# Performance work log

Measured on AMD Instinct MI355X. Metric: run time of the kernel, lower is better.

## Reference

```python
import jax, jax.numpy as jnp
import numpy as np

N_USER = 100000
N_ITEM = 100000
E = 1000000
D_IN = 64
D_OUT = 64


def setup_inputs() -> dict:
    key = jax.random.key(0)
    ks = jax.random.split(key, 10)
    scale = 1.0 / np.sqrt(D_IN)
    return {
        "feat_user": jax.random.normal(ks[0], (N_USER, D_IN), jnp.float32),
        "feat_item": jax.random.normal(ks[1], (N_ITEM, D_IN), jnp.float32),
        "src_clicks": jax.random.randint(ks[2], (E,), 0, N_USER),        # user ids
        "dst_clicks": jax.random.randint(ks[3], (E,), 0, N_ITEM),        # item ids
        "src_clicked_by": jax.random.randint(ks[4], (E,), 0, N_ITEM),    # item ids
        "dst_clicked_by": jax.random.randint(ks[5], (E,), 0, N_USER),    # user ids
        "W_clicks": jax.random.normal(ks[6], (D_OUT, D_IN), jnp.float32) * scale,
        "b_clicks": jax.random.normal(ks[7], (D_OUT,), jnp.float32) * scale,
        "W_clicked_by": jax.random.normal(ks[8], (D_OUT, D_IN), jnp.float32) * scale,
        "b_clicked_by": jax.random.normal(ks[9], (D_OUT,), jnp.float32) * scale,
    }


def _relation_mean(feat_src, W, b, src, dst, n_dst):
    # per-relation Linear on src features (nn.Linear: x @ W.T + b)
    Wh = feat_src @ W.T + b                                  # [N_src, D_OUT]
    # copy_u + mean: gather messages along edges, segment-mean at dst
    msum = jax.ops.segment_sum(Wh[src], dst, num_segments=n_dst)   # [n_dst, D_OUT]
    deg = jax.ops.segment_sum(jnp.ones(src.shape[0], jnp.float32), dst,
                              num_segments=n_dst)                   # [n_dst]
    return msum / jnp.maximum(deg, 1.0)[:, None]             # zero-degree dsts -> 0


def reference(feat_user, feat_item, src_clicks, dst_clicks,
              src_clicked_by, dst_clicked_by,
              W_clicks, b_clicks, W_clicked_by, b_clicked_by):
    # relation (user, clicks, item): messages land on item nodes
    h_item = _relation_mean(feat_user, W_clicks, b_clicks,
                            src_clicks, dst_clicks, N_ITEM)
    # relation (item, clicked_by, user): messages land on user nodes
    h_user = _relation_mean(feat_item, W_clicked_by, b_clicked_by,
                            src_clicked_by, dst_clicked_by, N_USER)
    # cross-relation 'sum' reducer: each ntype receives from exactly one relation here
    return (h_user, h_item)
```

## Files before the change

### kernel.cpp

```cpp
#include <hip/hip_runtime.h>

#define D 64
#define BSH 7
#define BK 128
#define NBK 1024
#define CAP 2048
#define CHUNK 4096
#define EPT (CHUNK / 256)
#define TILE 64

static __device__ __forceinline__ unsigned short f2bf(float x) {
    unsigned int u = __float_as_uint(x);
    unsigned int r = (u + 0x7FFFu + ((u >> 16) & 1u)) >> 16;
    return (unsigned short)r;
}
static __device__ __forceinline__ float bf2f(unsigned short h) {
    return __uint_as_float((unsigned int)h << 16);
}

__global__ __launch_bounds__(256) void linear_gemm(
    const float* __restrict__ feat_u, const float* __restrict__ feat_i,
    const float* __restrict__ W_c, const float* __restrict__ b_c,
    const float* __restrict__ W_cb, const float* __restrict__ b_cb,
    unsigned short* __restrict__ Whb_u, unsigned short* __restrict__ Whb_i,
    int n_user, int n_item) {
    const float* feat; const float* W; const float* bia; unsigned short* out; int n;
    if (blockIdx.y == 0) { feat = feat_u; W = W_c;  bia = b_c;  out = Whb_u; n = n_user; }
    else                 { feat = feat_i; W = W_cb; bia = b_cb; out = Whb_i; n = n_item; }
    int row0 = blockIdx.x * TILE;
    if (row0 >= n) return;
    __shared__ float FT[TILE * D];
    __shared__ float WT[D * 68];
    int t = threadIdx.x;
    int lr = t >> 4;
    int k4 = (t & 15) * 4;
    #pragma unroll
    for (int it = 0; it < 4; ++it) {
        int r = lr + it * 16;
        int grow = row0 + r; if (grow > n - 1) grow = n - 1;
        float4 f = *(const float4*)(feat + (size_t)grow * D + k4);
        *(float4*)(FT + r * D + k4) = f;
        float4 w = *(const float4*)(W + r * D + k4);
        WT[(k4 + 0) * 68 + r] = w.x;
        WT[(k4 + 1) * 68 + r] = w.y;
        WT[(k4 + 2) * 68 + r] = w.z;
        WT[(k4 + 3) * 68 + r] = w.w;
    }
    __syncthreads();
    int c0 = (t & 15) * 4;
    int r0 = (t >> 4) * 4;
    float4 bv = *(const float4*)(bia + c0);
    float acc[4][4];
    #pragma unroll
    for (int ri = 0; ri < 4; ++ri) {
        acc[ri][0] = bv.x; acc[ri][1] = bv.y; acc[ri][2] = bv.z; acc[ri][3] = bv.w;
    }
    #pragma unroll 4
    for (int k = 0; k < D; ++k) {
        float4 w = *(const float4*)(WT + k * 68 + c0);
        float f0 = FT[(r0 + 0) * D + k];
        float f1 = FT[(r0 + 1) * D + k];
        float f2 = FT[(r0 + 2) * D + k];
        float f3 = FT[(r0 + 3) * D + k];
        acc[0][0] = fmaf(f0, w.x, acc[0][0]); acc[0][1] = fmaf(f0, w.y, acc[0][1]);
        acc[0][2] = fmaf(f0, w.z, acc[0][2]); acc[0][3] = fmaf(f0, w.w, acc[0][3]);
        acc[1][0] = fmaf(f1, w.x, acc[1][0]); acc[1][1] = fmaf(f1, w.y, acc[1][1]);
        acc[1][2] = fmaf(f1, w.z, acc[1][2]); acc[1][3] = fmaf(f1, w.w, acc[1][3]);
        acc[2][0] = fmaf(f2, w.x, acc[2][0]); acc[2][1] = fmaf(f2, w.y, acc[2][1]);
        acc[2][2] = fmaf(f2, w.z, acc[2][2]); acc[2][3] = fmaf(f2, w.w, acc[2][3]);
        acc[3][0] = fmaf(f3, w.x, acc[3][0]); acc[3][1] = fmaf(f3, w.y, acc[3][1]);
        acc[3][2] = fmaf(f3, w.z, acc[3][2]); acc[3][3] = fmaf(f3, w.w, acc[3][3]);
    }
    #pragma unroll
    for (int ri = 0; ri < 4; ++ri) {
        int row = row0 + r0 + ri;
        if (row < n) {
            ushort4 o;
            o.x = f2bf(acc[ri][0]); o.y = f2bf(acc[ri][1]);
            o.z = f2bf(acc[ri][2]); o.w = f2bf(acc[ri][3]);
            *(ushort4*)(out + (size_t)row * D + c0) = o;
        }
    }
}

__global__ __launch_bounds__(256) void bucket_fill(
    const int* __restrict__ srcA, const int* __restrict__ dstA,
    const int* __restrict__ srcB, const int* __restrict__ dstB,
    int* __restrict__ bcur,
    unsigned int* __restrict__ ebufA, unsigned int* __restrict__ ebufB,
    int n_edges) {
    int rel = blockIdx.y;
    const int* src = rel ? srcB : srcA;
    const int* dst = rel ? dstB : dstA;
    int* bu = bcur + rel * NBK;
    unsigned int* ebuf = rel ? ebufB : ebufA;
    __shared__ int hist[NBK], lofs[NBK], lcur[NBK], runb[NBK];
    __shared__ unsigned int stage[CHUNK];
    __shared__ unsigned short sbkt[CHUNK];
    __shared__ int ps[256];
    int t = threadIdx.x;
    for (int i = t; i < NBK; i += 256) hist[i] = 0;
    __syncthreads();
    int base = blockIdx.x * CHUNK;
    int m = n_edges - base; if (m > CHUNK) m = CHUNK;
    unsigned int packed[EPT];
    int bk[EPT];
    #pragma unroll
    for (int j = 0; j < EPT; ++j) {
        int e = base + j * 256 + t;
        if (e < n_edges) {
            int d = dst[e];
            int s = src[e];
            bk[j] = ((unsigned)d) >> BSH;
            packed[j] = (unsigned int)s | (((unsigned int)d & (BK - 1)) << 24);
            atomicAdd(&hist[bk[j]], 1);
        } else bk[j] = -1;
    }
    __syncthreads();
    int a[4]; int s4 = 0;
    #pragma unroll
    for (int j = 0; j < 4; ++j) { a[j] = hist[4 * t + j]; s4 += a[j]; }
    ps[t] = s4;
    __syncthreads();
    for (int o = 1; o < 256; o <<= 1) {
        int x = (t >= o) ? ps[t - o] : 0;
        __syncthreads();
        ps[t] += x;
        __syncthreads();
    }
    int ex = ps[t] - s4;
    #pragma unroll
    for (int j = 0; j < 4; ++j) {
        lofs[4 * t + j] = ex; lcur[4 * t + j] = ex;
        ex += a[j];
    }
    __syncthreads();
    for (int b = t; b < NBK; b += 256) {
        int c = hist[b];
        runb[b] = c ? (b * CAP + atomicAdd(&bu[b], c)) : 0;
    }
    #pragma unroll
    for (int j = 0; j < EPT; ++j) {
        if (bk[j] >= 0) {
            int p = atomicAdd(&lcur[bk[j]], 1);
            stage[p] = packed[j];
            sbkt[p] = (unsigned short)bk[j];
        }
    }
    __syncthreads();
    for (int i = t; i < m; i += 256) {
        int b = sbkt[i];
        int pos = runb[b] + (i - lofs[b]);
        if ((unsigned)(pos - b * CAP) < CAP)
            ebuf[pos] = stage[i];
    }
}

__global__ __launch_bounds__(256) void bucket_gather(
    const unsigned short* __restrict__ Whb_u, const unsigned short* __restrict__ Whb_i,
    const unsigned int* __restrict__ ebufA, const unsigned int* __restrict__ ebufB,
    const int* __restrict__ bcur,
    float* __restrict__ h_user, float* __restrict__ h_item,
    int n_user, int n_item) {
    int rel = blockIdx.y;
    const unsigned short* Wh = rel ? Whb_u : Whb_i;
    const unsigned int* ebuf = rel ? ebufB : ebufA;
    float* out = rel ? h_item : h_user;
    int n = rel ? n_item : n_user;
    int b = blockIdx.x;
    int cnt = bcur[rel * NBK + b]; if (cnt > CAP) cnt = CAP;
    size_t base = (size_t)b * CAP;
    __shared__ unsigned int ssrc[CAP];
    __shared__ int hist[BK], ofs[BK], cur[BK];
    int t = threadIdx.x;
    if (t < BK) hist[t] = 0;
    __syncthreads();
    unsigned int pk[CAP / 256];
    #pragma unroll
    for (int j = 0; j < CAP / 256; ++j) {
        int i = t + j * 256;
        if (i < cnt) {
            pk[j] = ebuf[base + i];
            atomicAdd(&hist[pk[j] >> 24], 1);
        }
    }
    __syncthreads();
    if (t < BK) ofs[t] = hist[t];
    __syncthreads();
    for (int o = 1; o < BK; o <<= 1) {
        int x = (t >= o && t < BK) ? ofs[t - o] : 0;
        __syncthreads();
        if (t < BK) ofs[t] += x;
        __syncthreads();
    }
    if (t < BK) { int ex = ofs[t] - hist[t]; ofs[t] = ex; cur[t] = ex; }
    __syncthreads();
    #pragma unroll
    for (int j = 0; j < CAP / 256; ++j) {
        int i = t + j * 256;
        if (i < cnt) {
            int nd = pk[j] >> 24;
            int p = atomicAdd(&cur[nd], 1);
            ssrc[p] = pk[j] & 0xFFFFFFu;
        }
    }
    __syncthreads();
    int lane = t & 63;
    int w = t >> 6;
    int node0 = b * BK;
    for (int nd = w; nd < BK; nd += 4) {
        int node = node0 + nd;
        if (node >= n) break;
        int st = ofs[nd];
        int dg = hist[nd];
        int en = st + dg;
        float a0 = 0.f, a1 = 0.f;
        int j = st;
        for (; j + 1 < en; j += 2) {
            int s0 = ssrc[j];
            int s1 = ssrc[j + 1];
            a0 += bf2f(Wh[(size_t)s0 * D + lane]);
            a1 += bf2f(Wh[(size_t)s1 * D + lane]);
        }
        if (j < en) a0 += bf2f(Wh[(size_t)ssrc[j] * D + lane]);
        out[(size_t)node * D + lane] = (a0 + a1) / fmaxf((float)dg, 1.0f);
    }
}

extern "C" void kernel_launch(void* const* d_in, const int* in_sizes, int n_in,
                              void* d_out, int out_size, void* d_ws, size_t ws_size,
                              hipStream_t stream) {
    const float* feat_user      = (const float*)d_in[0];
    const float* feat_item      = (const float*)d_in[1];
    const int*   src_clicks     = (const int*)d_in[2];
    const int*   dst_clicks     = (const int*)d_in[3];
    const int*   src_clicked_by = (const int*)d_in[4];
    const int*   dst_clicked_by = (const int*)d_in[5];
    const float* W_clicks       = (const float*)d_in[6];
    const float* b_clicks       = (const float*)d_in[7];
    const float* W_clicked_by   = (const float*)d_in[8];
    const float* b_clicked_by   = (const float*)d_in[9];

    const int n_user  = in_sizes[0] / D;
    const int n_item  = in_sizes[1] / D;
    const int n_edges = in_sizes[2];

    float* out = (float*)d_out;
    float* h_user = out;
    float* h_item = out + (size_t)n_user * D;

    unsigned short* Whb_user = (unsigned short*)d_ws;
    unsigned short* Whb_item = Whb_user + (size_t)n_user * D;
    int* ip        = (int*)(Whb_item + (size_t)n_item * D);
    unsigned int* ebuf_user = (unsigned int*)ip;  ip += NBK * CAP;
    unsigned int* ebuf_item = (unsigned int*)ip;  ip += NBK * CAP;
    int* bcur = ip;

    hipMemsetAsync(bcur, 0, 2 * NBK * sizeof(int), stream);

    int ntile = (max(n_user, n_item) + TILE - 1) / TILE;
    linear_gemm<<<dim3(ntile, 2), 256, 0, stream>>>(
        feat_user, feat_item, W_clicks, b_clicks, W_clicked_by, b_clicked_by,
        Whb_user, Whb_item, n_user, n_item);

    int eb = (n_edges + CHUNK - 1) / CHUNK;
    bucket_fill<<<dim3(eb, 2), 256, 0, stream>>>(
        src_clicked_by, dst_clicked_by, src_clicks, dst_clicks,
        bcur, ebuf_user, ebuf_item, n_edges);

    int nbkt = (max(n_user, n_item) + BK - 1) / BK;
    bucket_gather<<<dim3(nbkt, 2), 256, 0, stream>>>(
        Whb_user, Whb_item, ebuf_user, ebuf_item, bcur,
        h_user, h_item, n_user, n_item);
}
```

Baseline: 238.6 us.

## Merge linear and bucket-fill into one launch; vectorize bf16 gather loads

The GEMM and edge-bucketing kernels become a single launch whose block ranges dispatch to either task, with shared memory held in a union. Because the two phases are independent, they can now overlap on the device and one launch boundary disappears. The gather loop changes from one bf16 per lane per edge to 32-bit loads: each half-wavefront handles alternate edges, four edges are in flight per iteration, and the two halves are combined with a cross-lane shuffle. The union forces the larger bucket-fill footprint on the GEMM blocks, which may lower their occupancy.

After: 231.9 us. 2.8% less time.

```diff
diff --git a/kernel.cpp b/kernel.cpp
--- a/kernel.cpp
+++ b/kernel.cpp
@@ -14,145 +14,148 @@
     unsigned int r = (u + 0x7FFFu + ((u >> 16) & 1u)) >> 16;
     return (unsigned short)r;
 }
-static __device__ __forceinline__ float bf2f(unsigned short h) {
-    return __uint_as_float((unsigned int)h << 16);
-}
-
-__global__ __launch_bounds__(256) void linear_gemm(
+
+__global__ __launch_bounds__(256) void phase1(
     const float* __restrict__ feat_u, const float* __restrict__ feat_i,
     const float* __restrict__ W_c, const float* __restrict__ b_c,
     const float* __restrict__ W_cb, const float* __restrict__ b_cb,
     unsigned short* __restrict__ Whb_u, unsigned short* __restrict__ Whb_i,
-    int n_user, int n_item) {
-    const float* feat; const float* W; const float* bia; unsigned short* out; int n;
-    if (blockIdx.y == 0) { feat = feat_u; W = W_c;  bia = b_c;  out = Whb_u; n = n_user; }
-    else                 { feat = feat_i; W = W_cb; bia = b_cb; out = Whb_i; n = n_item; }
-    int row0 = blockIdx.x * TILE;
-    if (row0 >= n) return;
-    __shared__ float FT[TILE * D];
-    __shared__ float WT[D * 68];
-    int t = threadIdx.x;
-    int lr = t >> 4;
-    int k4 = (t & 15) * 4;
-    #pragma unroll
-    for (int it = 0; it < 4; ++it) {
-        int r = lr + it * 16;
-        int grow = row0 + r; if (grow > n - 1) grow = n - 1;
-        float4 f = *(const float4*)(feat + (size_t)grow * D + k4);
-        *(float4*)(FT + r * D + k4) = f;
-        float4 w = *(const float4*)(W + r * D + k4);
-        WT[(k4 + 0) * 68 + r] = w.x;
-        WT[(k4 + 1) * 68 + r] = w.y;
-        WT[(k4 + 2) * 68 + r] = w.z;
-        WT[(k4 + 3) * 68 + r] = w.w;
-    }
-    __syncthreads();
-    int c0 = (t & 15) * 4;
-    int r0 = (t >> 4) * 4;
-    float4 bv = *(const float4*)(bia + c0);
-    float acc[4][4];
-    #pragma unroll
-    for (int ri = 0; ri < 4; ++ri) {
-        acc[ri][0] = bv.x; acc[ri][1] = bv.y; acc[ri][2] = bv.z; acc[ri][3] = bv.w;
-    }
-    #pragma unroll 4
-    for (int k = 0; k < D; ++k) {
-        float4 w = *(const float4*)(WT + k * 68 + c0);
-        float f0 = FT[(r0 + 0) * D + k];
-        float f1 = FT[(r0 + 1) * D + k];
-        float f2 = FT[(r0 + 2) * D + k];
-        float f3 = FT[(r0 + 3) * D + k];
-        acc[0][0] = fmaf(f0, w.x, acc[0][0]); acc[0][1] = fmaf(f0, w.y, acc[0][1]);
-        acc[0][2] = fmaf(f0, w.z, acc[0][2]); acc[0][3] = fmaf(f0, w.w, acc[0][3]);
-        acc[1][0] = fmaf(f1, w.x, acc[1][0]); acc[1][1] = fmaf(f1, w.y, acc[1][1]);
-        acc[1][2] = fmaf(f1, w.z, acc[1][2]); acc[1][3] = fmaf(f1, w.w, acc[1][3]);
-        acc[2][0] = fmaf(f2, w.x, acc[2][0]); acc[2][1] = fmaf(f2, w.y, acc[2][1]);
-        acc[2][2] = fmaf(f2, w.z, acc[2][2]); acc[2][3] = fmaf(f2, w.w, acc[2][3]);
-        acc[3][0] = fmaf(f3, w.x, acc[3][0]); acc[3][1] = fmaf(f3, w.y, acc[3][1]);
-        acc[3][2] = fmaf(f3, w.z, acc[3][2]); acc[3][3] = fmaf(f3, w.w, acc[3][3]);
-    }
-    #pragma unroll
-    for (int ri = 0; ri < 4; ++ri) {
-        int row = row0 + r0 + ri;
-        if (row < n) {
-            ushort4 o;
-            o.x = f2bf(acc[ri][0]); o.y = f2bf(acc[ri][1]);
-            o.z = f2bf(acc[ri][2]); o.w = f2bf(acc[ri][3]);
-            *(ushort4*)(out + (size_t)row * D + c0) = o;
-        }
-    }
-}
-
-__global__ __launch_bounds__(256) void bucket_fill(
     const int* __restrict__ srcA, const int* __restrict__ dstA,
     const int* __restrict__ srcB, const int* __restrict__ dstB,
     int* __restrict__ bcur,
     unsigned int* __restrict__ ebufA, unsigned int* __restrict__ ebufB,
-    int n_edges) {
-    int rel = blockIdx.y;
-    const int* src = rel ? srcB : srcA;
-    const int* dst = rel ? dstB : dstA;
-    int* bu = bcur + rel * NBK;
-    unsigned int* ebuf = rel ? ebufB : ebufA;
-    __shared__ int hist[NBK], lofs[NBK], lcur[NBK], runb[NBK];
-    __shared__ unsigned int stage[CHUNK];
-    __shared__ unsigned short sbkt[CHUNK];
-    __shared__ int ps[256];
+    int n_user, int n_item, int n_edges, int ntile, int eb) {
+    __shared__ union {
+        struct { float FT[TILE * D]; float WT[D * 68]; } lin;
+        struct { int hist[NBK], lofs[NBK], lcur[NBK], runb[NBK];
+                 unsigned int stage[CHUNK]; unsigned short sbkt[CHUNK];
+                 int ps[256]; } fil;
+    } sh;
     int t = threadIdx.x;
-    for (int i = t; i < NBK; i += 256) hist[i] = 0;
-    __syncthreads();
-    int base = blockIdx.x * CHUNK;
-    int m = n_edges - base; if (m > CHUNK) m = CHUNK;
-    unsigned int packed[EPT];
-    int bk[EPT];
-    #pragma unroll
-    for (int j = 0; j < EPT; ++j) {
-        int e = base + j * 256 + t;
-        if (e < n_edges) {
-            int d = dst[e];
-            int s = src[e];
-            bk[j] = ((unsigned)d) >> BSH;
-            packed[j] = (unsigned int)s | (((unsigned int)d & (BK - 1)) << 24);
-            atomicAdd(&hist[bk[j]], 1);
-        } else bk[j] = -1;
-    }
-    __syncthreads();
-    int a[4]; int s4 = 0;
-    #pragma unroll
-    for (int j = 0; j < 4; ++j) { a[j] = hist[4 * t + j]; s4 += a[j]; }
-    ps[t] = s4;
-    __syncthreads();
-    for (int o = 1; o < 256; o <<= 1) {
-        int x = (t >= o) ? ps[t - o] : 0;
-        __syncthreads();
-        ps[t] += x;
-        __syncthreads();
-    }
-    int ex = ps[t] - s4;
-    #pragma unroll
-    for (int j = 0; j < 4; ++j) {
-        lofs[4 * t + j] = ex; lcur[4 * t + j] = ex;
-        ex += a[j];
-    }
-    __syncthreads();
-    for (int b = t; b < NBK; b += 256) {
-        int c = hist[b];
-        runb[b] = c ? (b * CAP + atomicAdd(&bu[b], c)) : 0;
-    }
-    #pragma unroll
-    for (int j = 0; j < EPT; ++j) {
-        if (bk[j] >= 0) {
-            int p = atomicAdd(&lcur[bk[j]], 1);
-            stage[p] = packed[j];
-            sbkt[p] = (unsigned short)bk[j];
-        }
-    }
-    __syncthreads();
-    for (int i = t; i < m; i += 256) {
-        int b = sbkt[i];
-        int pos = runb[b] + (i - lofs[b]);
-        if ((unsigned)(pos - b * CAP) < CAP)
-            ebuf[pos] = stage[i];
+    int blk = blockIdx.x;
+
+    if (blk < 2 * ntile) {
+        int rel = (blk >= ntile);
+        int tile = rel ? blk - ntile : blk;
+        const float* feat = rel ? feat_i : feat_u;
+        const float* W    = rel ? W_cb   : W_c;
+        const float* bia  = rel ? b_cb   : b_c;
+        unsigned short* out = rel ? Whb_i : Whb_u;
+        int n = rel ? n_item : n_user;
+        int row0 = tile * TILE;
+        if (row0 >= n) return;
+        int lr = t >> 4;
+        int k4 = (t & 15) * 4;
+        #pragma unroll
+        for (int it = 0; it < 4; ++it) {
+            int r = lr + it * 16;
+            int grow = row0 + r; if (grow > n - 1) grow = n - 1;
+            float4 f = *(const float4*)(feat + (size_t)grow * D + k4);
+            *(float4*)(sh.lin.FT + r * D + k4) = f;
+            float4 w = *(const float4*)(W + r * D + k4);
+            sh.lin.WT[(k4 + 0) * 68 + r] = w.x;
+            sh.lin.WT[(k4 + 1) * 68 + r] = w.y;
+            sh.lin.WT[(k4 + 2) * 68 + r] = w.z;
+            sh.lin.WT[(k4 + 3) * 68 + r] = w.w;
+        }
+        __syncthreads();
+        int c0 = (t & 15) * 4;
+        int r0 = (t >> 4) * 4;
+        float4 bv = *(const float4*)(bia + c0);
+        float acc[4][4];
+        #pragma unroll
+        for (int ri = 0; ri < 4; ++ri) {
+            acc[ri][0] = bv.x; acc[ri][1] = bv.y; acc[ri][2] = bv.z; acc[ri][3] = bv.w;
+        }
+        #pragma unroll 4
+        for (int k = 0; k < D; ++k) {
+            float4 w = *(const float4*)(sh.lin.WT + k * 68 + c0);
+            float f0 = sh.lin.FT[(r0 + 0) * D + k];
+            float f1 = sh.lin.FT[(r0 + 1) * D + k];
+            float f2 = sh.lin.FT[(r0 + 2) * D + k];
+            float f3 = sh.lin.FT[(r0 + 3) * D + k];
+            acc[0][0] = fmaf(f0, w.x, acc[0][0]); acc[0][1] = fmaf(f0, w.y, acc[0][1]);
+            acc[0][2] = fmaf(f0, w.z, acc[0][2]); acc[0][3] = fmaf(f0, w.w, acc[0][3]);
+            acc[1][0] = fmaf(f1, w.x, acc[1][0]); acc[1][1] = fmaf(f1, w.y, acc[1][1]);
+            acc[1][2] = fmaf(f1, w.z, acc[1][2]); acc[1][3] = fmaf(f1, w.w, acc[1][3]);
+            acc[2][0] = fmaf(f2, w.x, acc[2][0]); acc[2][1] = fmaf(f2, w.y, acc[2][1]);
+            acc[2][2] = fmaf(f2, w.z, acc[2][2]); acc[2][3] = fmaf(f2, w.w, acc[2][3]);
+            acc[3][0] = fmaf(f3, w.x, acc[3][0]); acc[3][1] = fmaf(f3, w.y, acc[3][1]);
+            acc[3][2] = fmaf(f3, w.z, acc[3][2]); acc[3][3] = fmaf(f3, w.w, acc[3][3]);
+        }
+        #pragma unroll
+        for (int ri = 0; ri < 4; ++ri) {
+            int row = row0 + r0 + ri;
+            if (row < n) {
+                ushort4 o;
+                o.x = f2bf(acc[ri][0]); o.y = f2bf(acc[ri][1]);
+                o.z = f2bf(acc[ri][2]); o.w = f2bf(acc[ri][3]);
+                *(ushort4*)(out + (size_t)row * D + c0) = o;
+            }
+        }
+    } else {
+        int fb = blk - 2 * ntile;
+        int rel = (fb >= eb);
+        int chunk = rel ? fb - eb : fb;
+        const int* src = rel ? srcB : srcA;
+        const int* dst = rel ? dstB : dstA;
+        int* bu = bcur + rel * NBK;
+        unsigned int* ebuf = rel ? ebufB : ebufA;
+        for (int i = t; i < NBK; i += 256) sh.fil.hist[i] = 0;
+        __syncthreads();
+        int base = chunk * CHUNK;
+        int m = n_edges - base; if (m > CHUNK) m = CHUNK;
+        unsigned int packed[EPT];
+        int bk[EPT];
+        #pragma unroll
+        for (int j = 0; j < EPT; ++j) {
+            int e = base + j * 256 + t;
+            if (e < n_edges) {
+                int d = dst[e];
+                int s = src[e];
+                bk[j] = ((unsigned)d) >> BSH;
+                packed[j] = (unsigned int)s | (((unsigned int)d & (BK - 1)) << 24);
+                atomicAdd(&sh.fil.hist[bk[j]], 1);
+            } else bk[j] = -1;
+        }
+        __syncthreads();
+        int a[4]; int s4 = 0;
+        #pragma unroll
+        for (int j = 0; j < 4; ++j) { a[j] = sh.fil.hist[4 * t + j]; s4 += a[j]; }
+        sh.fil.ps[t] = s4;
+        __syncthreads();
+        for (int o = 1; o < 256; o <<= 1) {
+            int x = (t >= o) ? sh.fil.ps[t - o] : 0;
+            __syncthreads();
+            sh.fil.ps[t] += x;
+            __syncthreads();
+        }
+        int ex = sh.fil.ps[t] - s4;
+        #pragma unroll
+        for (int j = 0; j < 4; ++j) {
+            sh.fil.lofs[4 * t + j] = ex; sh.fil.lcur[4 * t + j] = ex;
+            ex += a[j];
+        }
+        __syncthreads();
+        for (int b = t; b < NBK; b += 256) {
+            int c = sh.fil.hist[b];
+            sh.fil.runb[b] = c ? (b * CAP + atomicAdd(&bu[b], c)) : 0;
+        }
+        #pragma unroll
+        for (int j = 0; j < EPT; ++j) {
+            if (bk[j] >= 0) {
+                int p = atomicAdd(&sh.fil.lcur[bk[j]], 1);
+                sh.fil.stage[p] = packed[j];
+                sh.fil.sbkt[p] = (unsigned short)bk[j];
+            }
+        }
+        __syncthreads();
+        for (int i = t; i < m; i += 256) {
+            int b = sh.fil.sbkt[i];
+            int pos = sh.fil.runb[b] + (i - sh.fil.lofs[b]);
+            if ((unsigned)(pos - b * CAP) < CAP)
+                ebuf[pos] = sh.fil.stage[i];
+        }
     }
 }
 
@@ -207,6 +210,8 @@
     __syncthreads();
     int lane = t & 63;
     int w = t >> 6;
+    int half = lane >> 5;
+    int lp = lane & 31;
     int node0 = b * BK;
     for (int nd = w; nd < BK; nd += 4) {
         int node = node0 + nd;
@@ -214,16 +219,29 @@
         int st = ofs[nd];
         int dg = hist[nd];
         int en = st + dg;
-        float a0 = 0.f, a1 = 0.f;
-        int j = st;
-        for (; j + 1 < en; j += 2) {
-            int s0 = ssrc[j];
-            int s1 = ssrc[j + 1];
-            a0 += bf2f(Wh[(size_t)s0 * D + lane]);
-            a1 += bf2f(Wh[(size_t)s1 * D + lane]);
-        }
-        if (j < en) a0 += bf2f(Wh[(size_t)ssrc[j] * D + lane]);
-        out[(size_t)node * D + lane] = (a0 + a1) / fmaxf((float)dg, 1.0f);
+        float l0 = 0.f, l1 = 0.f, l2 = 0.f, l3 = 0.f;
+        float h0 = 0.f, h1 = 0.f, h2 = 0.f, h3 = 0.f;
+        for (int j = st; j < en; j += 8) {
+            int e0 = j + 0 + half, e1 = j + 2 + half, e2 = j + 4 + half, e3 = j + 6 + half;
+            unsigned int v0 = 0, v1 = 0, v2 = 0, v3 = 0;
+            if (e0 < en) v0 = ((const unsigned int*)(Wh + (size_t)ssrc[e0] * D))[lp];
+            if (e1 < en) v1 = ((const unsigned int*)(Wh + (size_t)ssrc[e1] * D))[lp];
+            if (e2 < en) v2 = ((const unsigned int*)(Wh + (size_t)ssrc[e2] * D))[lp];
+            if (e3 < en) v3 = ((const unsigned int*)(Wh + (size_t)ssrc[e3] * D))[lp];
+            l0 += __uint_as_float(v0 << 16); h0 += __uint_as_float(v0 & 0xFFFF0000u);
+            l1 += __uint_as_float(v1 << 16); h1 += __uint_as_float(v1 & 0xFFFF0000u);
+            l2 += __uint_as_float(v2 << 16); h2 += __uint_as_float(v2 & 0xFFFF0000u);
+            l3 += __uint_as_float(v3 << 16); h3 += __uint_as_float(v3 & 0xFFFF0000u);
+        }
+        float lo = (l0 + l1) + (l2 + l3);
+        float hi = (h0 + h1) + (h2 + h3);
+        lo += __shfl_xor(lo, 32, 64);
+        hi += __shfl_xor(hi, 32, 64);
+        if (half == 0) {
+            float inv = 1.f / fmaxf((float)dg, 1.f);
+            float2 o; o.x = lo * inv; o.y = hi * inv;
+            *(float2*)(out + (size_t)node * D + 2 * lp) = o;
+        }
     }
 }
 
@@ -259,14 +277,13 @@
     hipMemsetAsync(bcur, 0, 2 * NBK * sizeof(int), stream);
 
     int ntile = (max(n_user, n_item) + TILE - 1) / TILE;
-    linear_gemm<<<dim3(ntile, 2), 256, 0, stream>>>(
+    int eb = (n_edges + CHUNK - 1) / CHUNK;
+    phase1<<<2 * ntile + 2 * eb, 256, 0, stream>>>(
         feat_user, feat_item, W_clicks, b_clicks, W_clicked_by, b_clicked_by,
-        Whb_user, Whb_item, n_user, n_item);
-
-    int eb = (n_edges + CHUNK - 1) / CHUNK;
-    bucket_fill<<<dim3(eb, 2), 256, 0, stream>>>(
+        Whb_user, Whb_item,
         src_clicked_by, dst_clicked_by, src_clicks, dst_clicks,
-        bcur, ebuf_user, ebuf_item, n_edges);
+        bcur, ebuf_user, ebuf_item,
+        n_user, n_item, n_edges, ntile, eb);
 
     int nbkt = (max(n_user, n_item) + BK - 1) / BK;
     bucket_gather<<<dim3(nbkt, 2), 256, 0, stream>>>(
```
